# Optimization experiments

Measured on AMD Instinct MI355X. Metric: run time of the kernel, lower is better.

The kernel has to match this reference:

```python
import jax, jax.numpy as jnp
import numpy as np

N, E = 20000, 320000
IN_DIM, H, C, L = 256, 128, 40, 3
EPS = 1e-5


def _ln(x, g, b):
    mu = jnp.mean(x, axis=-1, keepdims=True)
    var = jnp.mean(jnp.square(x - mu), axis=-1, keepdims=True)
    return (x - mu) * jax.lax.rsqrt(var + EPS) * g + b


def setup_inputs() -> dict:
    key = jax.random.key(0)
    ks = jax.random.split(key, 24)
    s = lambda *sh: 1.0 / np.sqrt(sh[-2] if len(sh) > 1 else sh[-1])
    inp = {
        "x": jax.random.normal(ks[0], (N, IN_DIM), jnp.float32),
        "edge_index": jax.random.randint(ks[1], (2, E), 0, N, jnp.int32),
        "proj_W": jax.random.normal(ks[2], (IN_DIM, H), jnp.float32) / np.sqrt(IN_DIM),
        "proj_b": jnp.zeros((H,), jnp.float32),
        "ln0_g": jnp.ones((H,), jnp.float32),
        "ln0_b": jnp.zeros((H,), jnp.float32),
        "sim_W1": jax.random.normal(ks[3], (L, 3 * H, H), jnp.float32) / np.sqrt(3 * H),
        "sim_b1": jnp.zeros((L, H), jnp.float32),
        "sim_W2": jax.random.normal(ks[4], (L, H, 1), jnp.float32) / np.sqrt(H),
        "sim_b2": jnp.zeros((L, 1), jnp.float32),
        "W_msg": jax.random.normal(ks[5], (L, H, H), jnp.float32) / np.sqrt(H),
        "W_upd": jax.random.normal(ks[6], (L, 2 * H, H), jnp.float32) / np.sqrt(2 * H),
        "b_upd": jnp.zeros((L, H), jnp.float32),
        "ln_g": jnp.ones((L, H), jnp.float32),
        "ln_b": jnp.zeros((L, H), jnp.float32),
        "cls_W1": jax.random.normal(ks[7], (H, H // 2), jnp.float32) / np.sqrt(H),
        "cls_b1": jnp.zeros((H // 2,), jnp.float32),
        "cls_W2": jax.random.normal(ks[8], (H // 2, C), jnp.float32) / np.sqrt(H // 2),
        "cls_b2": jnp.zeros((C,), jnp.float32),
    }
    return inp


def reference(x, edge_index, proj_W, proj_b, ln0_g, ln0_b, sim_W1, sim_b1,
              sim_W2, sim_b2, W_msg, W_upd, b_upd, ln_g, ln_b,
              cls_W1, cls_b1, cls_W2, cls_b2):
    n = x.shape[0]
    # add self loops
    loops = jnp.arange(n, dtype=edge_index.dtype)
    src = jnp.concatenate([edge_index[0], loops])
    dst = jnp.concatenate([edge_index[1], loops])

    h = jax.nn.relu(_ln(x @ proj_W + proj_b, ln0_g, ln0_b))  # (N,H); dropout=eval no-op

    for l in range(L):
        x_i = h[dst]                      # (E',H)
        x_j = h[src]                      # (E',H)
        sim_in = jnp.concatenate([x_i, x_j, jnp.abs(x_i - x_j)], axis=-1)  # (E',3H)
        hmid = jax.nn.relu(sim_in @ sim_W1[l] + sim_b1[l])
        score = jax.nn.sigmoid(hmid @ sim_W2[l] + sim_b2[l])  # (E',1)
        msg = x_j @ W_msg[l]              # (E',H)
        agg = jax.ops.segment_sum(score * msg, dst, num_segments=n)  # (N,H)
        upd = jnp.concatenate([h, agg], axis=-1) @ W_upd[l] + b_upd[l]
        upd = upd + h                     # residual (identity since in==out)
        h = jax.nn.relu(_ln(upd, ln_g[l], ln_b[l]))

    logits = jax.nn.relu(h @ cls_W1 + cls_b1) @ cls_W2 + cls_b2
    return logits
```

## Files before the change

### kernel.cpp

```cpp
#include <hip/hip_runtime.h>
#include <hip/hip_bf16.h>

#define HD 128
#define LN_EPS 1e-5f

typedef __attribute__((ext_vector_type(8))) short short8;
typedef __attribute__((ext_vector_type(4))) float f32x4;

__device__ __forceinline__ unsigned short f2bf(float f) {
    union { float f; unsigned u; } v; v.f = f;
    unsigned r = (v.u + 0x7fffu + ((v.u >> 16) & 1u)) >> 16;
    return (unsigned short)r;
}

__device__ __forceinline__ unsigned cvtpk(float lo, float hi) {
    unsigned r;
    asm("v_cvt_pk_bf16_f32 %0, %1, %2" : "=v"(r) : "v"(lo), "v"(hi));
    return r;
}
__device__ __forceinline__ unsigned cvtpk_abs(float lo, float hi) {
    unsigned r;
    asm("v_cvt_pk_bf16_f32 %0, abs(%1), abs(%2)" : "=v"(r) : "v"(lo), "v"(hi));
    return r;
}
__device__ __forceinline__ unsigned absd_bf2(unsigned a, unsigned b) {
    float alo = __uint_as_float(a << 16), ahi = __uint_as_float(a & 0xffff0000u);
    float blo = __uint_as_float(b << 16), bhi = __uint_as_float(b & 0xffff0000u);
    return cvtpk_abs(alo - blo, ahi - bhi);
}

__device__ __forceinline__ float wave_sum_all(float v) {
    #pragma unroll
    for (int o = 32; o > 0; o >>= 1) v += __shfl_xor(v, o);
    return v;
}

__global__ __launch_bounds__(256) void w1bf_kernel(
    const float* __restrict__ W1, unsigned short* __restrict__ out, int total)
{
    int idx = blockIdx.x * 256 + threadIdx.x;
    if (idx >= total) return;
    int lw  = idx / 49152;
    int rem = idx - lw * 49152;
    int j  = rem & 7;
    int c  = (rem >> 3) & 15;
    int ks = (rem >> 7) & 3;
    int ct = (rem >> 9) & 7;
    int q  = rem >> 12;
    out[idx] = f2bf(W1[(size_t)lw * 49152 + (size_t)(q * 32 + ks * 8 + j) * 128 + ct * 16 + c]);
}

__global__ __launch_bounds__(256) void wcbf_kernel(
    const float* __restrict__ wcomb, unsigned short* __restrict__ out, int total)
{
    int idx = blockIdx.x * 256 + threadIdx.x;
    if (idx >= total) return;
    int lw  = idx >> 15;
    int rem = idx & 32767;
    int j  = rem & 7;
    int c  = (rem >> 3) & 15;
    int ks = (rem >> 7) & 3;
    int ct = (rem >> 9) & 7;
    int q  = rem >> 12;
    out[idx] = f2bf(wcomb[(size_t)lw * 32768 + (size_t)(q * 32 + ks * 8 + j) * 128 + ct * 16 + c]);
}

__global__ __launch_bounds__(256) void copy_upd_kernel(
    const float* __restrict__ W_upd, float* __restrict__ wcomb, int total)
{
    int idx = blockIdx.x * 256 + threadIdx.x;
    if (idx >= total) return;
    int l = idx / 16384, r = idx - l * 16384;
    wcomb[(size_t)l * 32768 + r] = W_upd[(size_t)l * 32768 + r];
}

__global__ __launch_bounds__(256) void gemm_rows_kernel(
    const float* __restrict__ in0, int s0, const float* __restrict__ in1, int s1,
    const float* __restrict__ W, const float* __restrict__ bias,
    const float* __restrict__ res, const float* __restrict__ g,
    const float* __restrict__ bln, float* __restrict__ out,
    unsigned* __restrict__ out_bf, int N)
{
    __shared__ __align__(16) float rows[4][8][256];
    int tid = threadIdx.x, wv = tid >> 6, lane = tid & 63;
    int rbase = (blockIdx.x * 4 + wv) * 8;
    if (rbase >= N) return;
    int K = in1 ? 256 : 128;
    int r = lane >> 3, seg = lane & 7;
    int row = min(rbase + r, N - 1);
    {
        const float4* p = (const float4*)(in0 + (size_t)row * s0 + seg * 16);
        float4* q = (float4*)&rows[wv][r][seg * 16];
        #pragma unroll
        for (int i = 0; i < 4; i++) q[i] = p[i];
        if (in1) {
            const float4* p1 = (const float4*)(in1 + (size_t)row * s1 + seg * 16);
            float4* q1 = (float4*)&rows[wv][r][128 + seg * 16];
            #pragma unroll
            for (int i = 0; i < 4; i++) q1[i] = p1[i];
        }
    }
    asm volatile("s_waitcnt lgkmcnt(0)" ::: "memory");
    float2 acc[8];
    float2 bv = make_float2(0.f, 0.f);
    if (bias) bv = *(const float2*)(bias + 2 * lane);
    #pragma unroll
    for (int t = 0; t < 8; t++) acc[t] = bv;
    for (int k = 0; k < K; k += 4) {
        float2 w0 = *(const float2*)(W + (size_t)(k + 0) * 128 + 2 * lane);
        float2 w1 = *(const float2*)(W + (size_t)(k + 1) * 128 + 2 * lane);
        float2 w2 = *(const float2*)(W + (size_t)(k + 2) * 128 + 2 * lane);
        float2 w3 = *(const float2*)(W + (size_t)(k + 3) * 128 + 2 * lane);
        #pragma unroll
        for (int t = 0; t < 8; t++) {
            float4 a = *(const float4*)&rows[wv][t][k];
            acc[t].x = fmaf(a.x, w0.x, acc[t].x); acc[t].y = fmaf(a.x, w0.y, acc[t].y);
            acc[t].x = fmaf(a.y, w1.x, acc[t].x); acc[t].y = fmaf(a.y, w1.y, acc[t].y);
            acc[t].x = fmaf(a.z, w2.x, acc[t].x); acc[t].y = fmaf(a.z, w2.y, acc[t].y);
            acc[t].x = fmaf(a.w, w3.x, acc[t].x); acc[t].y = fmaf(a.w, w3.y, acc[t].y);
        }
    }
    if (res) {
        #pragma unroll
        for (int t = 0; t < 8; t++) {
            int rw = rbase + t;
            if (rw < N) {
                float2 rv = *(const float2*)(res + (size_t)rw * 128 + 2 * lane);
                acc[t].x += rv.x; acc[t].y += rv.y;
            }
        }
    }
    if (g) {
        float2 gv = *(const float2*)(g + 2 * lane);
        float2 lv = *(const float2*)(bln + 2 * lane);
        #pragma unroll
        for (int t = 0; t < 8; t++) {
            int rw = rbase + t;
            if (rw >= N) break;
            float s  = wave_sum_all(acc[t].x + acc[t].y);
            float s2 = wave_sum_all(acc[t].x * acc[t].x + acc[t].y * acc[t].y);
            float mu = s * (1.f / 128.f);
            float var = s2 * (1.f / 128.f) - mu * mu;
            float rs = rsqrtf(var + LN_EPS);
            float2 y;
            y.x = fmaxf((acc[t].x - mu) * rs * gv.x + lv.x, 0.f);
            y.y = fmaxf((acc[t].y - mu) * rs * gv.y + lv.y, 0.f);
            *(float2*)(out + (size_t)rw * 128 + 2 * lane) = y;
            if (out_bf) out_bf[(size_t)rw * 64 + lane] = cvtpk(y.x, y.y);
        }
    } else {
        #pragma unroll
        for (int t = 0; t < 8; t++) {
            int rw = rbase + t;
            if (rw < N) *(float2*)(out + (size_t)rw * 128 + 2 * lane) = acc[t];
        }
    }
}

__global__ __launch_bounds__(256) void hist_kernel(
    const int* __restrict__ dstA, int* __restrict__ cnt, int E, int Etot)
{
    for (int e = blockIdx.x * 256 + threadIdx.x; e < Etot; e += gridDim.x * 256) {
        int di = (e < E) ? dstA[e] : (e - E);
        atomicAdd(&cnt[di], 1);
    }
}

__global__ __launch_bounds__(256) void scan_kernel(
    const int* __restrict__ cnt, int* __restrict__ rowptr, int* __restrict__ cursor,
    int N, int Etot)
{
    __shared__ int ls[256];
    int t = threadIdx.x;
    int chunk = (N + 255) / 256;
    int lo = t * chunk, hi = min(lo + chunk, N);
    int s = 0;
    for (int i = lo; i < hi; i++) s += cnt[i];
    ls[t] = s;
    __syncthreads();
    for (int off = 1; off < 256; off <<= 1) {
        int v = (t >= off) ? ls[t - off] : 0;
        __syncthreads();
        ls[t] += v;
        __syncthreads();
    }
    int run = ls[t] - s;
    for (int i = lo; i < hi; i++) {
        rowptr[i] = run; cursor[i] = run;
        run += cnt[i];
    }
    if (t == 0) rowptr[N] = Etot;
}

__global__ __launch_bounds__(256) void scatter_kernel(
    const int* __restrict__ srcA, const int* __restrict__ dstA,
    int* __restrict__ cursor, int* __restrict__ esrc, int* __restrict__ edst,
    int E, int Etot)
{
    for (int e = blockIdx.x * 256 + threadIdx.x; e < Etot; e += gridDim.x * 256) {
        int si = (e < E) ? srcA[e] : (e - E);
        int di = (e < E) ? dstA[e] : (e - E);
        int pos = atomicAdd(&cursor[di], 1);
        esrc[pos] = si;
        edst[pos] = di;
    }
}

__global__ __launch_bounds__(256, 3) void edge_mfma_kernel(
    const unsigned* __restrict__ hbf,
    const int* __restrict__ esrc, const int* __restrict__ edst,
    const unsigned short* __restrict__ w1bf, const float* __restrict__ b1,
    const float* __restrict__ W2, const float* __restrict__ b2p,
    float* __restrict__ score, int Etot)
{
    __shared__ __align__(16) short sim[3][64][128];
    __shared__ float pl[4][64];
    int tid = threadIdx.x, wv = tid >> 6, lane = tid & 63;
    char* simb = (char*)sim;

    short8 wf[12][2];
    {
        int ks = lane >> 4, c = lane & 15;
        #pragma unroll
        for (int q = 0; q < 12; q++)
            #pragma unroll
            for (int n = 0; n < 2; n++) {
                int ct = wv * 2 + n;
                wf[q][n] = *(const short8*)(w1bf + (size_t)(((q * 8 + ct) * 4 + ks) * 128 + c * 8));
            }
    }
    float b1x = b1[wv * 32 + (lane & 15)],  b1y = b1[wv * 32 + 16 + (lane & 15)];
    float w2x = W2[wv * 32 + (lane & 15)],  w2y = W2[wv * 32 + 16 + (lane & 15)];
    float b2 = b2p[0];

    int nb = gridDim.x;
    int swz = (blockIdx.x & 7) * (nb >> 3) + (blockIdx.x >> 3);
    int ntiles = (Etot + 63) >> 6;
    int t0 = (int)(((long long)ntiles * swz) / nb);
    int t1 = (int)(((long long)ntiles * (swz + 1)) / nb);
    if (t0 >= t1) return;

    int el = tid >> 2, seg = tid & 3;
    int e_cur = min((t0 << 6) + el, Etot - 1);
    int si = esrc[e_cur];
    int di = edst[e_cur];

    for (int tile = t0; tile < t1; tile++) {
        const uint4* xi = (const uint4*)(hbf + (size_t)di * 64 + seg * 16);
        const uint4* xj = (const uint4*)(hbf + (size_t)si * 64 + seg * 16);
        uint4 a0 = xi[0], b0 = xj[0];
        uint4 a1 = xi[1], b1v = xj[1];
        uint4 a2 = xi[2], b2v = xj[2];
        uint4 a3 = xi[3], b3v = xj[3];
        {
            int nt = (tile + 1 < t1) ? (tile + 1) : tile;
            int en = min((nt << 6) + el, Etot - 1);
            si = esrc[en];
            di = edst[en];
        }
        {
            int rowoff = el * 256, sw = (el & 7) << 4;
            uint4 d0, d1, d2, d3;
            d0.x = absd_bf2(a0.x, b0.x);  d0.y = absd_bf2(a0.y, b0.y);
            d0.z = absd_bf2(a0.z, b0.z);  d0.w = absd_bf2(a0.w, b0.w);
            d1.x = absd_bf2(a1.x, b1v.x); d1.y = absd_bf2(a1.y, b1v.y);
            d1.z = absd_bf2(a1.z, b1v.z); d1.w = absd_bf2(a1.w, b1v.w);
            d2.x = absd_bf2(a2.x, b2v.x); d2.y = absd_bf2(a2.y, b2v.y);
            d2.z = absd_bf2(a2.z, b2v.z); d2.w = absd_bf2(a2.w, b2v.w);
            d3.x = absd_bf2(a3.x, b3v.x); d3.y = absd_bf2(a3.y, b3v.y);
            d3.z = absd_bf2(a3.z, b3v.z); d3.w = absd_bf2(a3.w, b3v.w);
            int o0 = rowoff + ((seg * 64 +  0) ^ sw);
            int o1 = rowoff + ((seg * 64 + 16) ^ sw);
            int o2 = rowoff + ((seg * 64 + 32) ^ sw);
            int o3 = rowoff + ((seg * 64 + 48) ^ sw);
            *(uint4*)(simb + o0)         = a0;  *(uint4*)(simb + o1)         = a1;
            *(uint4*)(simb + o2)         = a2;  *(uint4*)(simb + o3)         = a3;
            *(uint4*)(simb + 16384 + o0) = b0;  *(uint4*)(simb + 16384 + o1) = b1v;
            *(uint4*)(simb + 16384 + o2) = b2v; *(uint4*)(simb + 16384 + o3) = b3v;
            *(uint4*)(simb + 32768 + o0) = d0;  *(uint4*)(simb + 32768 + o1) = d1;
            *(uint4*)(simb + 32768 + o2) = d2;  *(uint4*)(simb + 32768 + o3) = d3;
        }
        __syncthreads();
        f32x4 acc[4][2];
        #pragma unroll
        for (int m = 0; m < 4; m++)
            #pragma unroll
            for (int n = 0; n < 2; n++)
                #pragma unroll
                for (int r = 0; r < 4; r++) acc[m][n][r] = 0.f;
        __builtin_amdgcn_s_setprio(1);
        #pragma unroll
        for (int q = 0; q < 12; q++) {
            int third = q >> 2;
            int kin = ((q & 3) * 64 + (lane >> 4) * 16);
            short8 af[4];
            #pragma unroll
            for (int m = 0; m < 4; m++) {
                int elr = m * 16 + (lane & 15);
                int addr = third * 16384 + elr * 256 + (kin ^ ((elr & 7) << 4));
                af[m] = *(const short8*)(simb + addr);
            }
            #pragma unroll
            for (int m = 0; m < 4; m++)
                #pragma unroll
                for (int n = 0; n < 2; n++)
                    acc[m][n] = __builtin_amdgcn_mfma_f32_16x16x32_bf16(af[m], wf[q][n], acc[m][n], 0, 0, 0);
        }
        __builtin_amdgcn_s_setprio(0);
        int ebase = tile << 6;
        #pragma unroll
        for (int m = 0; m < 4; m++) {
            #pragma unroll
            for (int r = 0; r < 4; r++) {
                float v = fmaxf(acc[m][0][r] + b1x, 0.f) * w2x
                        + fmaxf(acc[m][1][r] + b1y, 0.f) * w2y;
                v += __shfl_xor(v, 1); v += __shfl_xor(v, 2);
                v += __shfl_xor(v, 4); v += __shfl_xor(v, 8);
                if ((lane & 15) == 0) pl[wv][m * 16 + (lane >> 4) * 4 + r] = v;
            }
        }
        __syncthreads();
        if (tid < 64) {
            int e = ebase + tid;
            if (e < Etot) {
                float z = pl[0][tid] + pl[1][tid] + pl[2][tid] + pl[3][tid] + b2;
                score[e] = 1.f / (1.f + __expf(-z));
            }
        }
    }
}

__global__ __launch_bounds__(256) void gather_kernel(
    const int* __restrict__ rowptr, const int* __restrict__ esrc,
    const float* __restrict__ score, const unsigned* __restrict__ hbf,
    unsigned* __restrict__ paggbf, int N)
{
    int nb = gridDim.x;
    int bid = blockIdx.x;
    int swz = (bid & 7) * (nb >> 3) + (bid >> 3);
    int wvi = threadIdx.x >> 6, lane = threadIdx.x & 63;
    int node = swz * 4 + wvi;
    if (node >= N) return;
    int p0 = rowptr[node], p1 = rowptr[node + 1];
    float2 a0 = make_float2(0.f, 0.f), a1 = a0, a2 = a0, a3 = a0;
    for (int base = p0; base < p1; base += 64) {
        int cnt = min(64, p1 - base);
        int sidx = 0; float sc = 0.f;
        if (lane < cnt) {
            sidx = esrc[base + lane];
            sc = score[base + lane];
        }
        int i = 0;
        for (; i + 4 <= cnt; i += 4) {
            float s0 = __shfl(sc, i),     s1 = __shfl(sc, i + 1);
            float s2 = __shfl(sc, i + 2), s3 = __shfl(sc, i + 3);
            int r0 = __shfl(sidx, i),     r1 = __shfl(sidx, i + 1);
            int r2 = __shfl(sidx, i + 2), r3 = __shfl(sidx, i + 3);
            unsigned u0 = hbf[(size_t)r0 * 64 + lane];
            unsigned u1 = hbf[(size_t)r1 * 64 + lane];
            unsigned u2 = hbf[(size_t)r2 * 64 + lane];
            unsigned u3 = hbf[(size_t)r3 * 64 + lane];
            a0.x = fmaf(s0, __uint_as_float(u0 << 16), a0.x);
            a0.y = fmaf(s0, __uint_as_float(u0 & 0xffff0000u), a0.y);
            a1.x = fmaf(s1, __uint_as_float(u1 << 16), a1.x);
            a1.y = fmaf(s1, __uint_as_float(u1 & 0xffff0000u), a1.y);
            a2.x = fmaf(s2, __uint_as_float(u2 << 16), a2.x);
            a2.y = fmaf(s2, __uint_as_float(u2 & 0xffff0000u), a2.y);
            a3.x = fmaf(s3, __uint_as_float(u3 << 16), a3.x);
            a3.y = fmaf(s3, __uint_as_float(u3 & 0xffff0000u), a3.y);
        }
        for (; i < cnt; i++) {
            float s = __shfl(sc, i);
            int rr = __shfl(sidx, i);
            unsigned u = hbf[(size_t)rr * 64 + lane];
            a0.x = fmaf(s, __uint_as_float(u << 16), a0.x);
            a0.y = fmaf(s, __uint_as_float(u & 0xffff0000u), a0.y);
        }
    }
    float ox = (a0.x + a1.x) + (a2.x + a3.x);
    float oy = (a0.y + a1.y) + (a2.y + a3.y);
    paggbf[(size_t)node * 64 + lane] = cvtpk(ox, oy);
}

__global__ __launch_bounds__(256, 3) void upd_mfma_kernel(
    const unsigned* __restrict__ hbf, const unsigned* __restrict__ paggbf,
    const float* __restrict__ hres,
    const unsigned short* __restrict__ wcbf,
    const float* __restrict__ bias, const float* __restrict__ g,
    const float* __restrict__ bln,
    float* __restrict__ hout, unsigned* __restrict__ hbf_out, int N)
{
    __shared__ float ps[4][64], pq[4][64];
    int tid = threadIdx.x, wv = tid >> 6, lane = tid & 63;
    int c = lane & 15, l16 = lane >> 4;
    int rbase = blockIdx.x * 64;
    if (rbase >= N) return;

    short8 wf[8][2];
    #pragma unroll
    for (int q = 0; q < 8; q++)
        #pragma unroll
        for (int n = 0; n < 2; n++) {
            int ct = wv * 2 + n;
            wf[q][n] = *(const short8*)(wcbf + (size_t)(((q * 8 + ct) * 4 + l16) * 128 + c * 8));
        }
    float g0  = g[wv * 32 + c],    g1  = g[wv * 32 + 16 + c];
    float lb0 = bln[wv * 32 + c],  lb1 = bln[wv * 32 + 16 + c];
    float bs0 = bias[wv * 32 + c], bs1 = bias[wv * 32 + 16 + c];

    f32x4 acc[4][2];
    #pragma unroll
    for (int m = 0; m < 4; m++)
        #pragma unroll
        for (int n = 0; n < 2; n++)
            #pragma unroll
            for (int r = 0; r < 4; r++) acc[m][n][r] = 0.f;

    int arow[4];
    #pragma unroll
    for (int m = 0; m < 4; m++) arow[m] = min(rbase + m * 16 + c, N - 1);

    #pragma unroll
    for (int q = 0; q < 8; q++) {
        const unsigned* src = (q < 4) ? hbf : paggbf;
        int qq = (q < 4) ? q : q - 4;
        short8 af[4];
        #pragma unroll
        for (int m = 0; m < 4; m++)
            af[m] = *(const short8*)(src + (size_t)arow[m] * 64 + qq * 16 + l16 * 4);
        #pragma unroll
        for (int m = 0; m < 4; m++)
            #pragma unroll
            for (int n = 0; n < 2; n++)
                acc[m][n] = __builtin_amdgcn_mfma_f32_16x16x32_bf16(af[m], wf[q][n], acc[m][n], 0, 0, 0);
    }

    #pragma unroll
    for (int m = 0; m < 4; m++) {
        #pragma unroll
        for (int r = 0; r < 4; r++) {
            int rit = m * 16 + l16 * 4 + r;
            int rowc = min(rbase + rit, N - 1);
            float v0 = acc[m][0][r] + bs0 + hres[(size_t)rowc * 128 + wv * 32 + c];
            float v1 = acc[m][1][r] + bs1 + hres[(size_t)rowc * 128 + wv * 32 + 16 + c];
            acc[m][0][r] = v0; acc[m][1][r] = v1;
            float s = v0 + v1, sq = v0 * v0 + v1 * v1;
            s  += __shfl_xor(s, 1);  s  += __shfl_xor(s, 2);  s  += __shfl_xor(s, 4);  s  += __shfl_xor(s, 8);
            sq += __shfl_xor(sq, 1); sq += __shfl_xor(sq, 2); sq += __shfl_xor(sq, 4); sq += __shfl_xor(sq, 8);
            if (c == 0) { ps[wv][rit] = s; pq[wv][rit] = sq; }
        }
    }
    __syncthreads();
    #pragma unroll
    for (int m = 0; m < 4; m++) {
        #pragma unroll
        for (int r = 0; r < 4; r++) {
            int rit = m * 16 + l16 * 4 + r;
            int row = rbase + rit;
            float s  = (ps[0][rit] + ps[1][rit]) + (ps[2][rit] + ps[3][rit]);
            float sq = (pq[0][rit] + pq[1][rit]) + (pq[2][rit] + pq[3][rit]);
            float mu = s * (1.f / 128.f);
            float var = sq * (1.f / 128.f) - mu * mu;
            float rs = rsqrtf(var + LN_EPS);
            float y0 = fmaxf((acc[m][0][r] - mu) * rs * g0 + lb0, 0.f);
            float y1 = fmaxf((acc[m][1][r] - mu) * rs * g1 + lb1, 0.f);
            float z0 = __shfl_xor(y0, 1);
            float z1 = __shfl_xor(y1, 1);
            if (row < N) {
                hout[(size_t)row * 128 + wv * 32 + c]      = y0;
                hout[(size_t)row * 128 + wv * 32 + 16 + c] = y1;
                if (!(lane & 1)) {
                    hbf_out[(size_t)row * 64 + wv * 16 + (c >> 1)]     = cvtpk(y0, z0);
                    hbf_out[(size_t)row * 64 + wv * 16 + 8 + (c >> 1)] = cvtpk(y1, z1);
                }
            }
        }
    }
}

__global__ __launch_bounds__(256) void cls_kernel(
    const float* __restrict__ hin, const float* __restrict__ W1,
    const float* __restrict__ b1, const float* __restrict__ W2,
    const float* __restrict__ b2, float* __restrict__ out, int N)
{
    __shared__ __align__(16) float w1[HD * 64];
    __shared__ __align__(16) float w2[64 * 40];
    __shared__ __align__(16) float hs[4][HD];
    __shared__ float ts[4][64];
    for (int i = threadIdx.x; i < HD * 64; i += 256) w1[i] = W1[i];
    for (int i = threadIdx.x; i < 64 * 40; i += 256) w2[i] = W2[i];
    int sub = threadIdx.x >> 6, t = threadIdx.x & 63;
    float b1j = b1[t];
    float b2j = (t < 40) ? b2[t] : 0.f;
    __syncthreads();
    for (int base = blockIdx.x * 4; base < N; base += gridDim.x * 4) {
        int i = base + sub; bool val = i < N;
        if (val) { hs[sub][t] = hin[(size_t)i * HD + t]; hs[sub][64 + t] = hin[(size_t)i * HD + 64 + t]; }
        __syncthreads();
        float acc = b1j;
        const float* hr = hs[sub];
        #pragma unroll 8
        for (int k = 0; k < HD; k += 4) {
            float4 hv = *(const float4*)(hr + k);
            acc = fmaf(hv.x, w1[(k + 0) * 64 + t], acc);
            acc = fmaf(hv.y, w1[(k + 1) * 64 + t], acc);
            acc = fmaf(hv.z, w1[(k + 2) * 64 + t], acc);
            acc = fmaf(hv.w, w1[(k + 3) * 64 + t], acc);
        }
        ts[sub][t] = fmaxf(acc, 0.f);
        __syncthreads();
        if (val && t < 40) {
            float o = b2j;
            const float* tr = ts[sub];
            #pragma unroll 8
            for (int k = 0; k < 64; k++) o = fmaf(tr[k], w2[k * 40 + t], o);
            out[(size_t)i * 40 + t] = o;
        }
        __syncthreads();
    }
}

extern "C" void kernel_launch(void* const* d_in, const int* in_sizes, int n_in,
                              void* d_out, int out_size, void* d_ws, size_t ws_size,
                              hipStream_t stream)
{
    const float* x      = (const float*)d_in[0];
    const int*   ei     = (const int*)d_in[1];
    const float* proj_W = (const float*)d_in[2];
    const float* proj_b = (const float*)d_in[3];
    const float* ln0_g  = (const float*)d_in[4];
    const float* ln0_b  = (const float*)d_in[5];
    const float* sim_W1 = (const float*)d_in[6];
    const float* sim_b1 = (const float*)d_in[7];
    const float* sim_W2 = (const float*)d_in[8];
    const float* sim_b2 = (const float*)d_in[9];
    const float* W_msg  = (const float*)d_in[10];
    const float* W_upd  = (const float*)d_in[11];
    const float* b_upd  = (const float*)d_in[12];
    const float* ln_g   = (const float*)d_in[13];
    const float* ln_b   = (const float*)d_in[14];
    const float* cls_W1 = (const float*)d_in[15];
    const float* cls_b1 = (const float*)d_in[16];
    const float* cls_W2 = (const float*)d_in[17];
    const float* cls_b2 = (const float*)d_in[18];

    int N = in_sizes[0] / 256;
    int E = in_sizes[1] / 2;
    int L = in_sizes[6] / (3 * HD * HD);
    int Etot = E + N;
    const int* srcA = ei;
    const int* dstA = ei + E;

    float* ws = (float*)d_ws;
    size_t nh = (size_t)N * HD;
    float* h      = ws;
    float* score  = h + nh;
    float* wcomb  = score + Etot + 64;
    unsigned* hbf    = (unsigned*)(wcomb + (size_t)L * 32768);
    unsigned* paggbf = hbf + nh / 2;
    unsigned short* w1bf = (unsigned short*)(paggbf + nh / 2);
    unsigned short* wcbf = w1bf + (size_t)L * 49152;
    int*   cnt    = (int*)(wcbf + (size_t)L * 32768);
    int*   rowptr = cnt + N;
    int*   cursor = rowptr + N + 1;
    int*   esrc   = cursor + N;
    int*   edst   = esrc + Etot;

    int gemm_blocks = (N + 31) / 32;

    hipMemsetAsync(cnt, 0, (size_t)N * sizeof(int), stream);
    hist_kernel<<<512, 256, 0, stream>>>(dstA, cnt, E, Etot);
    scan_kernel<<<1, 256, 0, stream>>>(cnt, rowptr, cursor, N, Etot);
    scatter_kernel<<<512, 256, 0, stream>>>(srcA, dstA, cursor, esrc, edst, E, Etot);

    int w1_total = L * 49152;
    w1bf_kernel<<<(w1_total + 255) / 256, 256, 0, stream>>>(sim_W1, w1bf, w1_total);

    int cp_total = L * 16384;
    copy_upd_kernel<<<(cp_total + 255) / 256, 256, 0, stream>>>(W_upd, wcomb, cp_total);
    for (int l = 0; l < L; l++) {
        gemm_rows_kernel<<<(128 + 31) / 32, 256, 0, stream>>>(
            W_msg + (size_t)l * 16384, 128, nullptr, 0,
            W_upd + (size_t)l * 32768 + 16384, nullptr, nullptr, nullptr, nullptr,
            wcomb + (size_t)l * 32768 + 16384, nullptr, 128);
    }
    int wc_total = L * 32768;
    wcbf_kernel<<<(wc_total + 255) / 256, 256, 0, stream>>>(wcomb, wcbf, wc_total);

    gemm_rows_kernel<<<gemm_blocks, 256, 0, stream>>>(x, 256, x + 128, 256, proj_W, proj_b,
                                                      nullptr, ln0_g, ln0_b, h, hbf, N);

    int gather_blocks = (N + 3) / 4;
    int upd_blocks = (N + 63) / 64;
    for (int l = 0; l < L; l++) {
        edge_mfma_kernel<<<768, 256, 0, stream>>>(hbf, esrc, edst,
                                                  w1bf + (size_t)l * 49152, sim_b1 + l * HD,
                                                  sim_W2 + l * HD, sim_b2 + l, score, Etot);
        gather_kernel<<<gather_blocks, 256, 0, stream>>>(rowptr, esrc, score, hbf, paggbf, N);
        upd_mfma_kernel<<<upd_blocks, 256, 0, stream>>>(hbf, paggbf, h,
                                                        wcbf + (size_t)l * 32768,
                                                        b_upd + l * HD, ln_g + l * HD, ln_b + l * HD,
                                                        h, hbf, N);
    }
    cls_kernel<<<768, 256, 0, stream>>>(h, cls_W1, cls_b1, cls_W2, cls_b2, (float*)d_out, N);
}
```

Before: 454.7 us.

## Widen gather loads to uint2 across half-waves and fuse weight prep kernels

The gather kernel now splits each wave into two halves that handle alternate edges, each lane loading 8 bytes (4 bf16 features) per neighbor, with the halves combined at the end by a cross-half shuffle. This halves the number of gather load instructions per edge and issues more neighbor rows in flight. Separately, the copy kernel plus three per-layer W_msg@W_upd launches are replaced by one batched GEMM kernel, and the bf16 packing reads W_upd directly. The cost is extra shuffles and zero-masked tail lanes, plus one final cross-half reduction.

```diff
diff --git a/kernel.cpp b/kernel.cpp
--- a/kernel.cpp
+++ b/kernel.cpp
@@ -28,6 +28,8 @@
     float blo = __uint_as_float(b << 16), bhi = __uint_as_float(b & 0xffff0000u);
     return cvtpk_abs(alo - blo, ahi - bhi);
 }
+__device__ __forceinline__ float bflo(unsigned u) { return __uint_as_float(u << 16); }
+__device__ __forceinline__ float bfhi(unsigned u) { return __uint_as_float(u & 0xffff0000u); }
 
 __device__ __forceinline__ float wave_sum_all(float v) {
     #pragma unroll
@@ -51,7 +53,8 @@
 }
 
 __global__ __launch_bounds__(256) void wcbf_kernel(
-    const float* __restrict__ wcomb, unsigned short* __restrict__ out, int total)
+    const float* __restrict__ W_upd, const float* __restrict__ wcomb2,
+    unsigned short* __restrict__ out, int total)
 {
     int idx = blockIdx.x * 256 + threadIdx.x;
     if (idx >= total) return;
@@ -62,16 +65,53 @@
     int ks = (rem >> 7) & 3;
     int ct = (rem >> 9) & 7;
     int q  = rem >> 12;
-    out[idx] = f2bf(wcomb[(size_t)lw * 32768 + (size_t)(q * 32 + ks * 8 + j) * 128 + ct * 16 + c]);
-}
-
-__global__ __launch_bounds__(256) void copy_upd_kernel(
-    const float* __restrict__ W_upd, float* __restrict__ wcomb, int total)
-{
-    int idx = blockIdx.x * 256 + threadIdx.x;
-    if (idx >= total) return;
-    int l = idx / 16384, r = idx - l * 16384;
-    wcomb[(size_t)l * 32768 + r] = W_upd[(size_t)l * 32768 + r];
+    int row = q * 32 + ks * 8 + j;
+    int col = ct * 16 + c;
+    float v = (row < 128) ? W_upd[(size_t)lw * 32768 + (size_t)row * 128 + col]
+                          : wcomb2[(size_t)lw * 16384 + (size_t)(row - 128) * 128 + col];
+    out[idx] = f2bf(v);
+}
+
+__global__ __launch_bounds__(256) void wmsg_gemm_kernel(
+    const float* __restrict__ W_msg, const float* __restrict__ W_upd,
+    float* __restrict__ wcomb2)
+{
+    __shared__ __align__(16) float rows[4][8][128];
+    int l   = blockIdx.x >> 2;
+    int blk = blockIdx.x & 3;
+    const float* A = W_msg + (size_t)l * 16384;
+    const float* W = W_upd + (size_t)l * 32768 + 16384;
+    float* out = wcomb2 + (size_t)l * 16384;
+    int tid = threadIdx.x, wv = tid >> 6, lane = tid & 63;
+    int rbase = (blk * 4 + wv) * 8;
+    int r = lane >> 3, seg = lane & 7;
+    {
+        const float2* p = (const float2*)(A + (size_t)(rbase + r) * 128 + seg * 16);
+        float2* q = (float2*)&rows[wv][r][seg * 16];
+        #pragma unroll
+        for (int i = 0; i < 8; i++) q[i] = p[i];
+    }
+    asm volatile("s_waitcnt lgkmcnt(0)" ::: "memory");
+    float2 acc[8];
+    #pragma unroll
+    for (int t = 0; t < 8; t++) acc[t] = make_float2(0.f, 0.f);
+    for (int k = 0; k < 128; k += 4) {
+        float2 w0 = *(const float2*)(W + (size_t)(k + 0) * 128 + 2 * lane);
+        float2 w1 = *(const float2*)(W + (size_t)(k + 1) * 128 + 2 * lane);
+        float2 w2 = *(const float2*)(W + (size_t)(k + 2) * 128 + 2 * lane);
+        float2 w3 = *(const float2*)(W + (size_t)(k + 3) * 128 + 2 * lane);
+        #pragma unroll
+        for (int t = 0; t < 8; t++) {
+            float4 a = *(const float4*)&rows[wv][t][k];
+            acc[t].x = fmaf(a.x, w0.x, acc[t].x); acc[t].y = fmaf(a.x, w0.y, acc[t].y);
+            acc[t].x = fmaf(a.y, w1.x, acc[t].x); acc[t].y = fmaf(a.y, w1.y, acc[t].y);
+            acc[t].x = fmaf(a.z, w2.x, acc[t].x); acc[t].y = fmaf(a.z, w2.y, acc[t].y);
+            acc[t].x = fmaf(a.w, w3.x, acc[t].x); acc[t].y = fmaf(a.w, w3.y, acc[t].y);
+        }
+    }
+    #pragma unroll
+    for (int t = 0; t < 8; t++)
+        *(float2*)(out + (size_t)(rbase + t) * 128 + 2 * lane) = acc[t];
 }
 
 __global__ __launch_bounds__(256) void gemm_rows_kernel(
@@ -342,7 +382,9 @@
     int node = swz * 4 + wvi;
     if (node >= N) return;
     int p0 = rowptr[node], p1 = rowptr[node + 1];
-    float2 a0 = make_float2(0.f, 0.f), a1 = a0, a2 = a0, a3 = a0;
+    int half = lane >> 5, l32 = lane & 31;
+    const uint2* hb2 = (const uint2*)hbf;
+    float4 c0 = make_float4(0.f, 0.f, 0.f, 0.f), c1 = c0, c2 = c0, c3 = c0;
     for (int base = p0; base < p1; base += 64) {
         int cnt = min(64, p1 - base);
         int sidx = 0; float sc = 0.f;
@@ -350,36 +392,45 @@
             sidx = esrc[base + lane];
             sc = score[base + lane];
         }
-        int i = 0;
-        for (; i + 4 <= cnt; i += 4) {
-            float s0 = __shfl(sc, i),     s1 = __shfl(sc, i + 1);
-            float s2 = __shfl(sc, i + 2), s3 = __shfl(sc, i + 3);
-            int r0 = __shfl(sidx, i),     r1 = __shfl(sidx, i + 1);
-            int r2 = __shfl(sidx, i + 2), r3 = __shfl(sidx, i + 3);
-            unsigned u0 = hbf[(size_t)r0 * 64 + lane];
-            unsigned u1 = hbf[(size_t)r1 * 64 + lane];
-            unsigned u2 = hbf[(size_t)r2 * 64 + lane];
-            unsigned u3 = hbf[(size_t)r3 * 64 + lane];
-            a0.x = fmaf(s0, __uint_as_float(u0 << 16), a0.x);
-            a0.y = fmaf(s0, __uint_as_float(u0 & 0xffff0000u), a0.y);
-            a1.x = fmaf(s1, __uint_as_float(u1 << 16), a1.x);
-            a1.y = fmaf(s1, __uint_as_float(u1 & 0xffff0000u), a1.y);
-            a2.x = fmaf(s2, __uint_as_float(u2 << 16), a2.x);
-            a2.y = fmaf(s2, __uint_as_float(u2 & 0xffff0000u), a2.y);
-            a3.x = fmaf(s3, __uint_as_float(u3 << 16), a3.x);
-            a3.y = fmaf(s3, __uint_as_float(u3 & 0xffff0000u), a3.y);
-        }
-        for (; i < cnt; i++) {
-            float s = __shfl(sc, i);
-            int rr = __shfl(sidx, i);
-            unsigned u = hbf[(size_t)rr * 64 + lane];
-            a0.x = fmaf(s, __uint_as_float(u << 16), a0.x);
-            a0.y = fmaf(s, __uint_as_float(u & 0xffff0000u), a0.y);
-        }
-    }
-    float ox = (a0.x + a1.x) + (a2.x + a3.x);
-    float oy = (a0.y + a1.y) + (a2.y + a3.y);
-    paggbf[(size_t)node * 64 + lane] = cvtpk(ox, oy);
+        for (int i = 0; i < cnt; i += 8) {
+            int j0 = i + 0 + half, j1 = i + 2 + half, j2 = i + 4 + half, j3 = i + 6 + half;
+            float s0 = __shfl(sc, j0), s1 = __shfl(sc, j1);
+            float s2 = __shfl(sc, j2), s3 = __shfl(sc, j3);
+            int r0 = __shfl(sidx, j0), r1 = __shfl(sidx, j1);
+            int r2 = __shfl(sidx, j2), r3 = __shfl(sidx, j3);
+            if (j0 >= cnt) s0 = 0.f;
+            if (j1 >= cnt) s1 = 0.f;
+            if (j2 >= cnt) s2 = 0.f;
+            if (j3 >= cnt) s3 = 0.f;
+            uint2 u0 = hb2[(size_t)r0 * 32 + l32];
+            uint2 u1 = hb2[(size_t)r1 * 32 + l32];
+            uint2 u2 = hb2[(size_t)r2 * 32 + l32];
+            uint2 u3 = hb2[(size_t)r3 * 32 + l32];
+            c0.x = fmaf(s0, bflo(u0.x), c0.x); c0.y = fmaf(s0, bfhi(u0.x), c0.y);
+            c0.z = fmaf(s0, bflo(u0.y), c0.z); c0.w = fmaf(s0, bfhi(u0.y), c0.w);
+            c1.x = fmaf(s1, bflo(u1.x), c1.x); c1.y = fmaf(s1, bfhi(u1.x), c1.y);
+            c1.z = fmaf(s1, bflo(u1.y), c1.z); c1.w = fmaf(s1, bfhi(u1.y), c1.w);
+            c2.x = fmaf(s2, bflo(u2.x), c2.x); c2.y = fmaf(s2, bfhi(u2.x), c2.y);
+            c2.z = fmaf(s2, bflo(u2.y), c2.z); c2.w = fmaf(s2, bfhi(u2.y), c2.w);
+            c3.x = fmaf(s3, bflo(u3.x), c3.x); c3.y = fmaf(s3, bfhi(u3.x), c3.y);
+            c3.z = fmaf(s3, bflo(u3.y), c3.z); c3.w = fmaf(s3, bfhi(u3.y), c3.w);
+        }
+    }
+    float4 t;
+    t.x = (c0.x + c1.x) + (c2.x + c3.x);
+    t.y = (c0.y + c1.y) + (c2.y + c3.y);
+    t.z = (c0.z + c1.z) + (c2.z + c3.z);
+    t.w = (c0.w + c1.w) + (c2.w + c3.w);
+    t.x += __shfl_xor(t.x, 32);
+    t.y += __shfl_xor(t.y, 32);
+    t.z += __shfl_xor(t.z, 32);
+    t.w += __shfl_xor(t.w, 32);
+    if (half == 0) {
+        uint2 o;
+        o.x = cvtpk(t.x, t.y);
+        o.y = cvtpk(t.z, t.w);
+        ((uint2*)paggbf)[(size_t)node * 32 + l32] = o;
+    }
 }
 
 __global__ __launch_bounds__(256, 3) void upd_mfma_kernel(
@@ -555,8 +606,8 @@
     size_t nh = (size_t)N * HD;
     float* h      = ws;
     float* score  = h + nh;
-    float* wcomb  = score + Etot + 64;
-    unsigned* hbf    = (unsigned*)(wcomb + (size_t)L * 32768);
+    float* wcomb2 = score + Etot + 64;
+    unsigned* hbf    = (unsigned*)(wcomb2 + (size_t)L * 16384);
     unsigned* paggbf = hbf + nh / 2;
     unsigned short* w1bf = (unsigned short*)(paggbf + nh / 2);
     unsigned short* wcbf = w1bf + (size_t)L * 49152;
@@ -576,16 +627,9 @@
     int w1_total = L * 49152;
     w1bf_kernel<<<(w1_total + 255) / 256, 256, 0, stream>>>(sim_W1, w1bf, w1_total);
 
-    int cp_total = L * 16384;
-    copy_upd_kernel<<<(cp_total + 255) / 256, 256, 0, stream>>>(W_upd, wcomb, cp_total);
-    for (int l = 0; l < L; l++) {
-        gemm_rows_kernel<<<(128 + 31) / 32, 256, 0, stream>>>(
-            W_msg + (size_t)l * 16384, 128, nullptr, 0,
-            W_upd + (size_t)l * 32768 + 16384, nullptr, nullptr, nullptr, nullptr,
-            wcomb + (size_t)l * 32768 + 16384, nullptr, 128);
-    }
+    wmsg_gemm_kernel<<<4 * L, 256, 0, stream>>>(W_msg, W_upd, wcomb2);
     int wc_total = L * 32768;
-    wcbf_kernel<<<(wc_total + 255) / 256, 256, 0, stream>>>(wcomb, wcbf, wc_total);
+    wcbf_kernel<<<(wc_total + 255) / 256, 256, 0, stream>>>(W_upd, wcomb2, wcbf, wc_total);
 
     gemm_rows_kernel<<<gemm_blocks, 256, 0, stream>>>(x, 256, x + 128, 256, proj_W, proj_b,
                                                       nullptr, ln0_g, ln0_b, h, hbf, N);
```

After: 420.7 us, median of 2. -7.5%, faster.
